# Kernel optimization log

Hardware: AMD Instinct MI355X
Metric: run time of the kernel (lower is better)

## Reference

```python
import jax, jax.numpy as jnp
import numpy as np

Z_DIM = 64
HIDDEN = 400
DATASET = 1000000
EPS = 0.01
S_STEPS = 20
T_STEPS = 5
LOG_2PI = float(np.log(2.0 * np.pi))


def setup_inputs() -> dict:
    key = jax.random.key(0)
    ks = jax.random.split(key, 10)
    B = 16384
    x = jax.random.uniform(ks[0], (B, 1, 28, 28), dtype=jnp.float32)
    indices = jax.random.randint(ks[1], (B,), 0, DATASET, dtype=jnp.int64)
    # MLP params (torch Linear convention: y = x @ W.T + b)
    W1 = jax.random.normal(ks[2], (HIDDEN, 784), dtype=jnp.float32) * 0.03
    b1 = jnp.zeros((HIDDEN,), dtype=jnp.float32)
    W21 = jax.random.normal(ks[3], (Z_DIM, HIDDEN), dtype=jnp.float32) * 0.05
    b21 = jnp.zeros((Z_DIM,), dtype=jnp.float32)
    W22 = jax.random.normal(ks[4], (Z_DIM, HIDDEN), dtype=jnp.float32) * 0.05
    b22 = jnp.zeros((Z_DIM,), dtype=jnp.float32)
    cached_samples = jax.random.normal(ks[5], (DATASET, Z_DIM), dtype=jnp.float32)
    # pre-drawn Langevin noise for all s+t steps
    noise = jax.random.normal(ks[6], (S_STEPS + T_STEPS, B, Z_DIM), dtype=jnp.float32)
    return {"x": x, "indices": indices, "K": 1, "W1": W1, "b1": b1,
            "W21": W21, "b21": b21, "W22": W22, "b22": b22,
            "cached_samples": cached_samples, "noise": noise}


def _encode(x, W1, b1, W21, b21, W22, b22):
    xf = x.reshape(-1, 784)
    h = jax.nn.relu(xf @ W1.T + b1)
    z_loc = h @ W21.T + b21
    z_scale = jnp.exp(h @ W22.T + b22)
    return z_loc, z_scale


def _langevin(z0, noise_steps, z_loc, z_scale):
    # ULA: z <- z + eps * grad_log_q(z) + sqrt(2*eps) * xi
    inv_var = 1.0 / (z_scale * z_scale)
    coef = jnp.sqrt(2.0 * EPS).astype(z0.dtype)

    def step(z, xi):
        grad = (z_loc - z) * inv_var
        return z + EPS * grad + coef * xi, None

    z, _ = jax.lax.scan(step, z0, noise_steps)
    return z


def reference(x, indices, K, W1, b1, W21, b21, W22, b22, cached_samples, noise):
    z_loc, z_scale = _encode(x, W1, b1, W21, b21, W22, b22)
    # gather cached particles
    z = cached_samples[indices]
    # s detached steps, then t graph-carrying steps (same math in fwd)
    z = jax.lax.stop_gradient(_langevin(z, noise[:S_STEPS], z_loc, z_scale))
    z = _langevin(z, noise[S_STEPS:], z_loc, z_scale)
    # scatter updated particles back
    new_cache = cached_samples.at[indices].set(jax.lax.stop_gradient(z))
    # Normal log-prob summed over latent dim
    log_qz_x = jnp.sum(
        -0.5 * jnp.square((z - z_loc) / z_scale) - jnp.log(z_scale) - 0.5 * LOG_2PI,
        axis=-1)
    return log_qz_x, z, new_cache
```

## Files before the change

kernel.cpp:

```cpp
#include <hip/hip_runtime.h>


#define ZD 64
#define NSTEPS 25
#define EPSI 0.01f
#define K1 784
#define K1P 800
#define HSTR 512

typedef __attribute__((ext_vector_type(8))) short short8;
typedef __attribute__((ext_vector_type(4))) float f32x4;
typedef __attribute__((ext_vector_type(4))) int i32x4;

__device__ __forceinline__ unsigned short f2bf(float f) {
  union { float f; unsigned u; } v; v.f = f;
  return (unsigned short)((v.u + 0x7FFFu + ((v.u >> 16) & 1u)) >> 16);
}

__device__ __forceinline__ void gload_lds16(const void* g, void* l) {
  __builtin_amdgcn_global_load_lds(
      (const __attribute__((address_space(1))) void*)g,
      (__attribute__((address_space(3))) void*)l, 16, 0, 0);
}

__global__ __launch_bounds__(256) void prep_kernel(
    const float* __restrict__ W1, const float* __restrict__ W21,
    const float* __restrict__ W22, short* __restrict__ W1b,
    short* __restrict__ Wout) {
  const int t = blockIdx.x * 256 + threadIdx.x;
  const int NW1 = 512 * (K1P / 8);
  if (t < NW1) {
    const int n = t / (K1P / 8), k0 = (t % (K1P / 8)) * 8;
    short8 v = {0, 0, 0, 0, 0, 0, 0, 0};
    if (n < 400 && k0 < K1) {
      const float* s = W1 + (long)n * K1 + k0;
#pragma unroll
      for (int e = 0; e < 8; e++) v[e] = (short)f2bf(s[e]);
    }
    *(short8*)(W1b + (long)t * 8) = v;
  } else {
    const int q = t - NW1;
    if (q < 128 * 64) {
      const int n = q / 64, k0 = (q % 64) * 8;
      short8 v = {0, 0, 0, 0, 0, 0, 0, 0};
      if (k0 < 400) {
        const float* s = (n < 64) ? (W21 + (long)n * 400 + k0)
                                  : (W22 + (long)(n - 64) * 400 + k0);
#pragma unroll
        for (int e = 0; e < 8; e++) v[e] = (short)f2bf(s[e]);
      }
      *(short8*)(Wout + (long)q * 8) = v;
    }
  }
}

__global__ __launch_bounds__(256) void zero_win_kernel(i32x4* __restrict__ win4, int n4) {
  const int t = blockIdx.x * 256 + threadIdx.x;
  if (t < n4) win4[t] = (i32x4){0, 0, 0, 0};
}

__global__ __launch_bounds__(256) void winner_kernel(
    const int* __restrict__ idx, int* __restrict__ winner, int B) {
  const int j = blockIdx.x * 256 + threadIdx.x;
  if (j < B) atomicMax(&winner[idx[j]], j + 1);
}

__global__ __launch_bounds__(256) void gemm1_kernel(
    const float* __restrict__ X, const short* __restrict__ W1b,
    const float* __restrict__ b1, unsigned short* __restrict__ H) {
  __shared__ short As[2 * 64 * 8];
  __shared__ short Bs[32 * 64 * 8];
  const int tid = threadIdx.x;
  const int w = tid >> 6;
  const int lane = tid & 63;
  const int m0 = blockIdx.x * 32;

  const f32x4 vzero = {0.f, 0.f, 0.f, 0.f};
  f32x4 acc[2][8];
#pragma unroll
  for (int i = 0; i < 2; i++)
#pragma unroll
    for (int j = 0; j < 8; j++) acc[i][j] = vzero;

  for (int k0 = 0; k0 < K1P; k0 += 32) {
    if (k0) __syncthreads();
    if (tid < 128) {
      const int row = m0 + (tid >> 6) * 16 + (lane & 15);
      const int gk = k0 + (lane >> 4) * 8;
      short8 av = {0, 0, 0, 0, 0, 0, 0, 0};
      if (gk < K1) {
        const float4 f0 = *(const float4*)(X + (long)row * K1 + gk);
        const float4 f1 = *(const float4*)(X + (long)row * K1 + gk + 4);
        av[0] = (short)f2bf(f0.x); av[1] = (short)f2bf(f0.y);
        av[2] = (short)f2bf(f0.z); av[3] = (short)f2bf(f0.w);
        av[4] = (short)f2bf(f1.x); av[5] = (short)f2bf(f1.y);
        av[6] = (short)f2bf(f1.z); av[7] = (short)f2bf(f1.w);
      }
      *(short8*)(As + (long)tid * 8) = av;
    }
#pragma unroll
    for (int t = 0; t < 8; t++) {
      const int gn = w * 8 + t;
      const short* src = W1b + (long)(gn * 16 + (lane & 15)) * K1P +
                         k0 + (lane >> 4) * 8;
      gload_lds16(src, Bs + gn * 512);
    }
    __syncthreads();
    const short8* Ap = (const short8*)As;
    const short8* Bp = (const short8*)Bs;
    const short8 a0 = Ap[0 * 64 + lane];
    const short8 a1 = Ap[1 * 64 + lane];
#pragma unroll
    for (int j = 0; j < 8; j++) {
      const short8 b = Bp[(w * 8 + j) * 64 + lane];
      acc[0][j] = __builtin_amdgcn_mfma_f32_16x16x32_bf16(a0, b, acc[0][j], 0, 0, 0);
      acc[1][j] = __builtin_amdgcn_mfma_f32_16x16x32_bf16(a1, b, acc[1][j], 0, 0, 0);
    }
  }
  const int colg = lane & 15;
  const int rowg = (lane >> 4) * 4;
#pragma unroll
  for (int j = 0; j < 8; j++) {
    const int col = w * 128 + j * 16 + colg;
    const float bias = (col < 400) ? b1[col] : 0.f;
#pragma unroll
    for (int i = 0; i < 2; i++) {
      const int rbase = m0 + i * 16 + rowg;
#pragma unroll
      for (int r = 0; r < 4; r++) {
        H[(long)(rbase + r) * HSTR + col] = f2bf(fmaxf(acc[i][j][r] + bias, 0.f));
      }
    }
  }
}

__global__ __launch_bounds__(256) void gemm2_kernel(
    const unsigned short* __restrict__ H, const short* __restrict__ Wout,
    const float* __restrict__ b21, const float* __restrict__ b22,
    float* __restrict__ zloc, float* __restrict__ uarr) {
  __shared__ short As[2 * 64 * 8];
  __shared__ short Bs[8 * 64 * 8];
  const int tid = threadIdx.x;
  const int w = tid >> 6;
  const int lane = tid & 63;
  const int m0 = blockIdx.x * 32;

  const f32x4 vzero = {0.f, 0.f, 0.f, 0.f};
  f32x4 acc[2][2];
#pragma unroll
  for (int i = 0; i < 2; i++)
#pragma unroll
    for (int j = 0; j < 2; j++) acc[i][j] = vzero;

  for (int k0 = 0; k0 < HSTR; k0 += 32) {
    if (k0) __syncthreads();
    if (w < 2) {
      const unsigned short* src = H + (long)(m0 + w * 16 + (lane & 15)) * HSTR +
                                  k0 + (lane >> 4) * 8;
      gload_lds16(src, As + w * 512);
    }
#pragma unroll
    for (int t = 0; t < 2; t++) {
      const int gn = w * 2 + t;
      const short* src = Wout + (long)(gn * 16 + (lane & 15)) * HSTR +
                         k0 + (lane >> 4) * 8;
      gload_lds16(src, Bs + gn * 512);
    }
    __syncthreads();
    const short8* Ap = (const short8*)As;
    const short8* Bp = (const short8*)Bs;
    const short8 a0 = Ap[0 * 64 + lane];
    const short8 a1 = Ap[1 * 64 + lane];
#pragma unroll
    for (int j = 0; j < 2; j++) {
      const short8 b = Bp[(w * 2 + j) * 64 + lane];
      acc[0][j] = __builtin_amdgcn_mfma_f32_16x16x32_bf16(a0, b, acc[0][j], 0, 0, 0);
      acc[1][j] = __builtin_amdgcn_mfma_f32_16x16x32_bf16(a1, b, acc[1][j], 0, 0, 0);
    }
  }
  const int colg = lane & 15;
  const int rowg = (lane >> 4) * 4;
  float* outp = (w < 2) ? zloc : uarr;
  const float* bp = (w < 2) ? b21 : b22;
#pragma unroll
  for (int j = 0; j < 2; j++) {
    const int col = (w & 1) * 32 + j * 16 + colg;
    const float bias = bp[col];
#pragma unroll
    for (int i = 0; i < 2; i++) {
      const int rbase = m0 + i * 16 + rowg;
#pragma unroll
      for (int r = 0; r < 4; r++) {
        outp[(long)(rbase + r) * ZD + col] = acc[i][j][r] + bias;
      }
    }
  }
}

__global__ __launch_bounds__(256) void langevin_kernel(
    const float* __restrict__ zloc, const float* __restrict__ uarr,
    const float* __restrict__ cache, const int* __restrict__ idx,
    const float* __restrict__ noise, float* __restrict__ out_logq,
    float* __restrict__ out_z, int B) {
  const int row = blockIdx.x * 4 + (threadIdx.x >> 6);
  const int lane = threadIdx.x & 63;
  const int i = idx[row];
  const float zl = zloc[(long)row * ZD + lane];
  const float uu = uarr[(long)row * ZD + lane];
  const float a = EPSI * expf(-2.f * uu);
  float z = cache[(long)i * ZD + lane];
  const float coef = sqrtf(2.f * EPSI);
  const float* np = noise + (long)row * ZD + lane;
  const long stride = (long)B * ZD;
#pragma unroll
  for (int s = 0; s < NSTEPS; s++) {
    z = z + a * (zl - z) + coef * np[(long)s * stride];
  }
  out_z[(long)row * ZD + lane] = z;
  const float d = (z - zl) * expf(-uu);
  float t = -0.5f * d * d - uu - 0.91893853320467274178f;
#pragma unroll
  for (int off = 1; off < 64; off <<= 1) t += __shfl_xor(t, off);
  if (lane == 0) out_logq[row] = t;
}

__global__ __launch_bounds__(256) void copy_kernel(
    const f32x4* __restrict__ cache4, const f32x4* __restrict__ z4,
    const int* __restrict__ winner, f32x4* __restrict__ out4) {
  const long e = (long)blockIdx.x * 256 + threadIdx.x;
  const long row = e >> 4;
  const int c = (int)(e & 15);
  const int w = winner[row];
  f32x4 v;
  if (w == 0) v = __builtin_nontemporal_load(&cache4[e]);
  else        v = z4[(long)(w - 1) * 16 + c];
  __builtin_nontemporal_store(v, &out4[e]);
}

extern "C" void kernel_launch(void* const* d_in, const int* in_sizes, int n_in,
                              void* d_out, int out_size, void* d_ws, size_t ws_size,
                              hipStream_t stream) {
  const float* x     = (const float*)d_in[0];
  const int*   idx   = (const int*)d_in[1];
  const float* W1    = (const float*)d_in[3];
  const float* b1    = (const float*)d_in[4];
  const float* W21   = (const float*)d_in[5];
  const float* b21   = (const float*)d_in[6];
  const float* W22   = (const float*)d_in[7];
  const float* b22   = (const float*)d_in[8];
  const float* cache = (const float*)d_in[9];
  const float* noise = (const float*)d_in[10];

  const int B  = in_sizes[1];
  const int DS = in_sizes[9] / ZD;

  float* out_logq  = (float*)d_out;
  float* out_z     = out_logq + B;
  float* out_cache = out_z + (long)B * ZD;

  unsigned short* h = (unsigned short*)d_ws;
  short* w1b  = (short*)(h + (long)B * HSTR);
  short* wout = w1b + 512 * K1P;
  float* zloc = (float*)(wout + 128 * HSTR);
  float* u    = zloc + (long)B * ZD;
  int*   win  = (int*)(u + (long)B * ZD);

  const int n4 = (DS + 3) / 4;
  zero_win_kernel<<<(n4 + 255) / 256, 256, 0, stream>>>((i32x4*)win, n4);

  const int prep_chunks = 512 * (K1P / 8) + 128 * 64;
  prep_kernel<<<(prep_chunks + 255) / 256, 256, 0, stream>>>(W1, W21, W22, w1b, wout);
  gemm1_kernel<<<B / 32, 256, 0, stream>>>(x, w1b, b1, h);
  gemm2_kernel<<<B / 32, 256, 0, stream>>>(h, wout, b21, b22, zloc, u);
  winner_kernel<<<(B + 255) / 256, 256, 0, stream>>>(idx, win, B);
  langevin_kernel<<<B / 4, 256, 0, stream>>>(zloc, u, cache, idx, noise,
                                             out_logq, out_z, B);
  const long total4 = (long)DS * (ZD / 4);
  copy_kernel<<<(unsigned)(total4 / 256), 256, 0, stream>>>(
      (const f32x4*)cache, (const f32x4*)out_z, win, (f32x4*)out_cache);
}
```

Measured before the change: 191.9 us.

## Overlap bulk cache copy with GEMM1 and scatter winners from Langevin kernel

The full cache copy (256 MB read plus 256 MB write) now runs as extra blocks inside the GEMM1 launch, so the memory-bound copy overlaps the compute-bound GEMM. The per-row winner lookup is removed from the copy. The Langevin kernel now writes each updated particle directly into the output cache, and only the last duplicate index writes, decided by the winner array. This drops one launch and the winner gather, but it relies on the copy blocks finishing before the Langevin scatter, which stream ordering guarantees. The copy blocks may compete with the GEMM for bandwidth and CU slots.

```diff
diff --git a/kernel.cpp b/kernel.cpp
--- a/kernel.cpp
+++ b/kernel.cpp
@@ -7,6 +7,7 @@
 #define K1 784
 #define K1P 800
 #define HSTR 512
+#define COPYB 2048
 
 typedef __attribute__((ext_vector_type(8))) short short8;
 typedef __attribute__((ext_vector_type(4))) float f32x4;
@@ -65,12 +66,28 @@
   if (j < B) atomicMax(&winner[idx[j]], j + 1);
 }
 
-__global__ __launch_bounds__(256) void gemm1_kernel(
+__global__ __launch_bounds__(256) void gemm1_copy_kernel(
     const float* __restrict__ X, const short* __restrict__ W1b,
-    const float* __restrict__ b1, unsigned short* __restrict__ H) {
+    const float* __restrict__ b1, unsigned short* __restrict__ H,
+    const f32x4* __restrict__ cache4, f32x4* __restrict__ out4,
+    int ngemm, long n4) {
   __shared__ short As[2 * 64 * 8];
   __shared__ short Bs[32 * 64 * 8];
   const int tid = threadIdx.x;
+
+  if ((int)blockIdx.x >= ngemm) {
+    const long base = (long)(blockIdx.x - ngemm) * (256 * 32) + tid;
+#pragma unroll
+    for (int k = 0; k < 32; k++) {
+      const long e = base + (long)k * 256;
+      if (e < n4) {
+        f32x4 v = __builtin_nontemporal_load(&cache4[e]);
+        __builtin_nontemporal_store(v, &out4[e]);
+      }
+    }
+    return;
+  }
+
   const int w = tid >> 6;
   const int lane = tid & 63;
   const int m0 = blockIdx.x * 32;
@@ -200,8 +217,9 @@
 __global__ __launch_bounds__(256) void langevin_kernel(
     const float* __restrict__ zloc, const float* __restrict__ uarr,
     const float* __restrict__ cache, const int* __restrict__ idx,
-    const float* __restrict__ noise, float* __restrict__ out_logq,
-    float* __restrict__ out_z, int B) {
+    const float* __restrict__ noise, const int* __restrict__ winner,
+    float* __restrict__ out_logq, float* __restrict__ out_z,
+    float* __restrict__ out_cache, int B) {
   const int row = blockIdx.x * 4 + (threadIdx.x >> 6);
   const int lane = threadIdx.x & 63;
   const int i = idx[row];
@@ -217,24 +235,14 @@
     z = z + a * (zl - z) + coef * np[(long)s * stride];
   }
   out_z[(long)row * ZD + lane] = z;
+  if (winner[i] == row + 1) {
+    out_cache[(long)i * ZD + lane] = z;
+  }
   const float d = (z - zl) * expf(-uu);
   float t = -0.5f * d * d - uu - 0.91893853320467274178f;
 #pragma unroll
   for (int off = 1; off < 64; off <<= 1) t += __shfl_xor(t, off);
   if (lane == 0) out_logq[row] = t;
-}
-
-__global__ __launch_bounds__(256) void copy_kernel(
-    const f32x4* __restrict__ cache4, const f32x4* __restrict__ z4,
-    const int* __restrict__ winner, f32x4* __restrict__ out4) {
-  const long e = (long)blockIdx.x * 256 + threadIdx.x;
-  const long row = e >> 4;
-  const int c = (int)(e & 15);
-  const int w = winner[row];
-  f32x4 v;
-  if (w == 0) v = __builtin_nontemporal_load(&cache4[e]);
-  else        v = z4[(long)(w - 1) * 16 + c];
-  __builtin_nontemporal_store(v, &out4[e]);
 }
 
 extern "C" void kernel_launch(void* const* d_in, const int* in_sizes, int n_in,
@@ -265,17 +273,19 @@
   float* u    = zloc + (long)B * ZD;
   int*   win  = (int*)(u + (long)B * ZD);
 
-  const int n4 = (DS + 3) / 4;
-  zero_win_kernel<<<(n4 + 255) / 256, 256, 0, stream>>>((i32x4*)win, n4);
+  const int n4i = (DS + 3) / 4;
+  zero_win_kernel<<<(n4i + 255) / 256, 256, 0, stream>>>((i32x4*)win, n4i);
 
   const int prep_chunks = 512 * (K1P / 8) + 128 * 64;
   prep_kernel<<<(prep_chunks + 255) / 256, 256, 0, stream>>>(W1, W21, W22, w1b, wout);
-  gemm1_kernel<<<B / 32, 256, 0, stream>>>(x, w1b, b1, h);
+  winner_kernel<<<(B + 255) / 256, 256, 0, stream>>>(idx, win, B);
+
+  const int ngemm = B / 32;
+  const long total4 = (long)DS * (ZD / 4);
+  gemm1_copy_kernel<<<ngemm + COPYB, 256, 0, stream>>>(
+      x, w1b, b1, h, (const f32x4*)cache, (f32x4*)out_cache, ngemm, total4);
+
   gemm2_kernel<<<B / 32, 256, 0, stream>>>(h, wout, b21, b22, zloc, u);
-  winner_kernel<<<(B + 255) / 256, 256, 0, stream>>>(idx, win, B);
-  langevin_kernel<<<B / 4, 256, 0, stream>>>(zloc, u, cache, idx, noise,
-                                             out_logq, out_z, B);
-  const long total4 = (long)DS * (ZD / 4);
-  copy_kernel<<<(unsigned)(total4 / 256), 256, 0, stream>>>(
-      (const f32x4*)cache, (const f32x4*)out_z, win, (f32x4*)out_cache);
-}
+  langevin_kernel<<<B / 4, 256, 0, stream>>>(zloc, u, cache, idx, noise, win,
+                                             out_logq, out_z, out_cache, B);
+}
```

Result: no change. 191.2 us (-0.4%).
